# Kernel tuning notes

Hardware: AMD Instinct MI355X
Metric: run time of the kernel (lower is better)

The kernel has to match this reference:

```python
import jax, jax.numpy as jnp
import numpy as np

B, C, H, W = 8, 512, 64, 64
R = 16
CQK = C // R  # 32


def setup_inputs() -> dict:
    key = jax.random.key(0)
    kx, kq, kk, kv = jax.random.split(key, 4)
    x = jax.random.normal(kx, (B, C, H, W), dtype=jnp.float32)
    # Conv1d with kernel_size=1, bias=False == matmul over channel dim
    Wq = jax.random.normal(kq, (CQK, C), dtype=jnp.float32) * (1.0 / np.sqrt(C))
    Wk = jax.random.normal(kk, (CQK, C), dtype=jnp.float32) * (1.0 / np.sqrt(C))
    Wv = jax.random.normal(kv, (C, C), dtype=jnp.float32) * (1.0 / np.sqrt(C))
    return {"x": x, "Wq": Wq, "Wk": Wk, "Wv": Wv}


def reference(x, Wq, Wk, Wv):
    b, c, h, w = x.shape
    xf = x.reshape(b, c, h * w)                 # [b, c, n]
    q = jnp.einsum('dc,bcn->bdn', Wq, xf)       # [b, c/r, n]
    k = jnp.einsum('dc,bcn->bdn', Wk, xf)       # [b, c/r, n]
    attn = jax.nn.softmax(jnp.einsum('bdm,bdn->bmn', q, k), axis=-1)  # [b, n, n]
    v = jnp.einsum('dc,bcn->bdn', Wv, xf)       # [b, c, n]
    out = jnp.einsum('bcm,bmn->bcn', v, attn)   # [b, c, n]
    return out.reshape(b, c, h, w)
```

## Files before the change

### kernel.cpp

```cpp
#include <hip/hip_runtime.h>
#include <hip/hip_bf16.h>


typedef __attribute__((ext_vector_type(8))) short s16x8;
typedef __attribute__((ext_vector_type(4))) float f32x4;

#define MFMA16(a, b, c) __builtin_amdgcn_mfma_f32_16x16x32_bf16((a), (b), (c), 0, 0, 0)

__device__ __forceinline__ ushort f2bf(float f) {
  union { float f; unsigned u; } v; v.f = f;
  return (ushort)((v.u + 0x8000u) >> 16);
}
__device__ __forceinline__ unsigned pack_bf16(float lo, float hi) {
  union { float f; unsigned u; } a, b; a.f = lo; b.f = hi;
  return __builtin_amdgcn_perm(b.u + 0x8000u, a.u + 0x8000u, 0x07060302u);
}
__device__ __forceinline__ float fexp2(float x) { return __builtin_amdgcn_exp2f(x); }

__device__ __forceinline__ void chunk_barrier() {
  asm volatile("s_waitcnt lgkmcnt(0)" ::: "memory");
  __builtin_amdgcn_s_barrier();
  __builtin_amdgcn_sched_barrier(0);
}

__global__ void k_cvt_w(const float* __restrict__ Wq, const float* __restrict__ Wk,
                        const float* __restrict__ Wv, ushort* __restrict__ Wqb,
                        ushort* __restrict__ Wkb, ushort* __restrict__ Wvb) {
  int i = blockIdx.x * 256 + threadIdx.x;
  if (i < 262144) Wvb[i] = f2bf(Wv[i]);
  else if (i < 278528) Wqb[i - 262144] = f2bf(Wq[i - 262144] * 1.4426950408889634f);
  else if (i < 294912) Wkb[i - 278528] = f2bf(Wk[i - 278528]);
}

__global__ __launch_bounds__(256) void k_xpose(const float* __restrict__ x,
                                               ushort* __restrict__ xT) {
  const int b = blockIdx.z, c0 = blockIdx.y * 64, n0 = blockIdx.x * 256;
  __shared__ uint U[2][64][65];
  const int t = threadIdx.x;
  const int wv = t >> 6, ln = t & 63;
  const float* xp = x + ((size_t)b * 512 + c0 + wv * 16) * 4096 + n0 + ln * 4;
#pragma unroll
  for (int i = 0; i < 16; ++i) {
    float4 f = *(const float4*)(xp + (size_t)i * 4096);
    U[0][wv * 16 + i][ln] = pack_bf16(f.x, f.y);
    U[1][wv * 16 + i][ln] = pack_bf16(f.z, f.w);
  }
  __syncthreads();
  const int c_seg = (t & 7) * 8;
#pragma unroll
  for (int pass = 0; pass < 8; ++pass) {
    const int nl = pass * 32 + (t >> 3);
    const int p = nl >> 1;
    const int h = p & 1, idx = p >> 1;
    const uint sel = (nl & 1) ? 0x07060302u : 0x05040100u;
    uint o[4];
#pragma unroll
    for (int j = 0; j < 4; ++j) {
      uint ua = U[h][c_seg + 2 * j][idx];
      uint ub = U[h][c_seg + 2 * j + 1][idx];
      o[j] = __builtin_amdgcn_perm(ub, ua, sel);
    }
    *(uint4*)(xT + ((size_t)b * 4096 + n0 + nl) * 512 + c0 + c_seg) = *(uint4*)o;
  }
}

__global__ __launch_bounds__(256, 2) void k_proj(const ushort* __restrict__ xT,
                                                 const ushort* __restrict__ Wqb,
                                                 const ushort* __restrict__ Wkb,
                                                 const ushort* __restrict__ Wvb,
                                                 ushort* __restrict__ qb,
                                                 ushort* __restrict__ kb,
                                                 ushort* __restrict__ vb) {
  const int b = blockIdx.y, n0 = blockIdx.x * 64;
  const int lane = threadIdx.x & 63, w = threadIdx.x >> 6;
  const int quad = lane >> 4, l15 = lane & 15;
  const ushort* xT_b = xT + (size_t)b * 4096 * 512;

  const ushort* Wqk = (w < 2) ? (Wqb + (size_t)(w * 16 + l15) * 512)
                              : (Wkb + (size_t)((w - 2) * 16 + l15) * 512);

  f32x4 accv[8][4], accqk[4];
#pragma unroll
  for (int i = 0; i < 8; ++i)
#pragma unroll
    for (int nt = 0; nt < 4; ++nt) accv[i][nt] = {0.f, 0.f, 0.f, 0.f};
#pragma unroll
  for (int nt = 0; nt < 4; ++nt) accqk[nt] = {0.f, 0.f, 0.f, 0.f};

  for (int k0 = 0; k0 < 512; k0 += 32) {
    s16x8 bx[4];
#pragma unroll
    for (int nt = 0; nt < 4; ++nt)
      bx[nt] = *(const s16x8*)(xT_b + (size_t)(n0 + nt * 16 + l15) * 512 + k0 + quad * 8);
#pragma unroll
    for (int i = 0; i < 8; ++i) {
      s16x8 av = *(const s16x8*)(Wvb + (size_t)((8 * w + i) * 16 + l15) * 512 + k0 + quad * 8);
#pragma unroll
      for (int nt = 0; nt < 4; ++nt) accv[i][nt] = MFMA16(av, bx[nt], accv[i][nt]);
    }
    s16x8 aqk = *(const s16x8*)(Wqk + k0 + quad * 8);
#pragma unroll
    for (int nt = 0; nt < 4; ++nt) accqk[nt] = MFMA16(aqk, bx[nt], accqk[nt]);
  }

  ushort* vb_b = vb + (size_t)b * 512 * 4096;
#pragma unroll
  for (int i = 0; i < 8; ++i)
#pragma unroll
    for (int nt = 0; nt < 4; ++nt)
#pragma unroll
      for (int r = 0; r < 4; ++r)
        vb_b[(size_t)((8 * w + i) * 16 + quad * 4 + r) * 4096 + n0 + nt * 16 + l15] =
            f2bf(accv[i][nt][r]);

  ushort* qk_out = (w < 2) ? (qb + (size_t)b * 4096 * 32) : (kb + (size_t)b * 4096 * 32);
#pragma unroll
  for (int nt = 0; nt < 4; ++nt) {
    ushort4 u;
    u.x = f2bf(accqk[nt][0]); u.y = f2bf(accqk[nt][1]);
    u.z = f2bf(accqk[nt][2]); u.w = f2bf(accqk[nt][3]);
    *(ushort4*)(qk_out + (size_t)(n0 + nt * 16 + l15) * 32 + (w & 1) * 16 + quad * 4) = u;
  }
}

__global__ __launch_bounds__(256) void k_pass1(const ushort* __restrict__ qb,
                                               const ushort* __restrict__ kb,
                                               float* __restrict__ Lneg) {
  const int b = blockIdx.y, mt = blockIdx.x;
  const int lane = threadIdx.x & 63, w = threadIdx.x >> 6;
  const int quad = lane >> 4, l15 = lane & 15;
  const int m = mt * 64 + w * 16;
  const ushort* qb_b = qb + (size_t)b * 4096 * 32;
  const ushort* kb_b = kb + (size_t)b * 4096 * 32;
  const s16x8 aqf = *(const s16x8*)(qb_b + (size_t)(m + l15) * 32 + quad * 8);
  float ps[4] = {0.f, 0.f, 0.f, 0.f};
  const f32x4 zf = {0.f, 0.f, 0.f, 0.f};
  for (int n0 = 0; n0 < 4096; n0 += 64) {
#pragma unroll
    for (int nt = 0; nt < 4; ++nt) {
      s16x8 bk = *(const s16x8*)(kb_b + (size_t)(n0 + nt * 16 + l15) * 32 + quad * 8);
      f32x4 s = MFMA16(aqf, bk, zf);
#pragma unroll
      for (int r = 0; r < 4; ++r) ps[r] += fexp2(s[r]);
    }
  }
  for (int off = 1; off < 16; off <<= 1)
#pragma unroll
    for (int r = 0; r < 4; ++r) ps[r] += __shfl_xor(ps[r], off, 64);
  if (l15 == 0)
#pragma unroll
    for (int r = 0; r < 4; ++r)
      Lneg[(size_t)b * 4096 + m + quad * 4 + r] = -log2f(ps[r]);
}

__global__ __launch_bounds__(512, 2) void k_pass2(const ushort* __restrict__ qb,
                                                  const ushort* __restrict__ kb,
                                                  const ushort* __restrict__ vb,
                                                  const float* __restrict__ Lneg,
                                                  float* __restrict__ out) {
  const int blk = blockIdx.x;
  const int b = blk & 7, ntb = blk >> 3;
  const int nbase = ntb * 128;
  const int lane = threadIdx.x & 63, w = threadIdx.x >> 6;
  const int quad = lane >> 4, l15 = lane & 15;
  const int cbase = w * 64;
  const int swz = l15 & 7;
  const int Mw = w >> 1;
  const int Tb = (w & 1) * 4;

  __shared__ __align__(16) ushort PT[2][128 * 64];

  const ushort* qb_b = qb + (size_t)b * 4096 * 32;
  const ushort* kb_b = kb + (size_t)b * 4096 * 32;
  const ushort* vb_b = vb + (size_t)b * 512 * 4096;
  const float* L_b = Lneg + (size_t)b * 4096;

  s16x8 kf[4];
#pragma unroll
  for (int i = 0; i < 4; ++i)
    kf[i] = *(const s16x8*)(kb_b + (size_t)(nbase + (Tb + i) * 16 + l15) * 32 + quad * 8);

  f32x4 acc[4][8];
#pragma unroll
  for (int ci = 0; ci < 4; ++ci)
#pragma unroll
    for (int nt = 0; nt < 8; ++nt) acc[ci][nt] = {0.f, 0.f, 0.f, 0.f};

  s16x8 aqp;
  float4 l4p;
  s16x8 va0[4], va1[4];

  auto loadQ = [&](int chunk) {
    const int m0 = chunk * 64;
    aqp = *(const s16x8*)(qb_b + (size_t)(m0 + Mw * 16 + l15) * 32 + quad * 8);
    l4p = *(const float4*)(L_b + m0 + Mw * 16 + quad * 4);
  };
  auto loadV0 = [&](int chunk) {
    const int m0 = chunk * 64;
#pragma unroll
    for (int ci = 0; ci < 4; ++ci)
      va0[ci] = *(const s16x8*)(vb_b + (size_t)(cbase + ci * 16 + l15) * 4096 + m0 + quad * 8);
  };
  auto loadV1 = [&](int chunk) {
    const int m0 = chunk * 64;
#pragma unroll
    for (int ci = 0; ci < 4; ++ci)
      va1[ci] = *(const s16x8*)(vb_b + (size_t)(cbase + ci * 16 + l15) * 4096 + m0 + 32 + quad * 8);
  };
  auto produce_tile = [&](int buf, int i) {
    char* Pw = (char*)&PT[buf][0];
    const int T = Tb + i;
    f32x4 cin; cin.x = l4p.x; cin.y = l4p.y; cin.z = l4p.z; cin.w = l4p.w;
    f32x4 s = MFMA16(aqp, kf[i], cin);
    uint2 u;
    u.x = pack_bf16(fexp2(s.x), fexp2(s.y));
    u.y = pack_bf16(fexp2(s.z), fexp2(s.w));
    const int row = T * 16 + l15;
    const int gran = (2 * Mw + (quad >> 1)) ^ swz;
    *(uint2*)(Pw + row * 128 + gran * 16 + (quad & 1) * 8) = u;
  };

  loadQ(0);
#pragma unroll
  for (int i = 0; i < 4; ++i) produce_tile(0, i);
  loadQ(1);
  loadV0(0);
  loadV1(0);

  for (int chunk = 0; chunk < 64; ++chunk) {
    const int buf = chunk & 1;
    chunk_barrier();
    const char* P = (const char*)&PT[buf][0];
    s16x8 pg[8];
#pragma unroll
    for (int nt = 0; nt < 8; ++nt)
      pg[nt] = *(const s16x8*)(P + (nt * 16 + l15) * 128 + (quad ^ swz) * 16);
#pragma unroll
    for (int i = 0; i < 4; ++i) produce_tile(buf ^ 1, i);
    if (chunk < 62) loadQ(chunk + 2);
    s16x8 rr[8];
#pragma unroll
    for (int nt = 0; nt < 8; ++nt) {
#pragma unroll
      for (int ci = 0; ci < 4; ++ci) acc[ci][nt] = MFMA16(va0[ci], pg[nt], acc[ci][nt]);
      rr[nt] = *(const s16x8*)(P + (nt * 16 + l15) * 128 + ((4 + quad) ^ swz) * 16);
    }
    if (chunk < 63) loadV0(chunk + 1);
#pragma unroll
    for (int nt = 0; nt < 8; ++nt)
#pragma unroll
      for (int ci = 0; ci < 4; ++ci) acc[ci][nt] = MFMA16(va1[ci], rr[nt], acc[ci][nt]);
    if (chunk < 63) loadV1(chunk + 1);
  }

  float* out_b = out + (size_t)b * 512 * 4096;
#pragma unroll
  for (int ci = 0; ci < 4; ++ci)
#pragma unroll
    for (int nt = 0; nt < 8; ++nt) {
      const int n = nbase + nt * 16 + l15;
      const int c0 = cbase + ci * 16 + quad * 4;
#pragma unroll
      for (int r = 0; r < 4; ++r) out_b[(size_t)(c0 + r) * 4096 + n] = acc[ci][nt][r];
    }
}

extern "C" void kernel_launch(void* const* d_in, const int* in_sizes, int n_in,
                              void* d_out, int out_size, void* d_ws, size_t ws_size,
                              hipStream_t stream) {
  const float* x  = (const float*)d_in[0];
  const float* Wq = (const float*)d_in[1];
  const float* Wk = (const float*)d_in[2];
  const float* Wv = (const float*)d_in[3];
  float* out = (float*)d_out;

  char* ws = (char*)d_ws;
  ushort* vb  = (ushort*)(ws + 0);
  ushort* xT  = (ushort*)(ws + 33554432);
  ushort* qb  = (ushort*)(ws + 67108864);
  ushort* kb  = (ushort*)(ws + 69206016);
  ushort* Wvb = (ushort*)(ws + 71303168);
  ushort* Wqb = (ushort*)(ws + 71827456);
  ushort* Wkb = (ushort*)(ws + 71860224);
  float*  Lrs = (float*)(ws + 71892992);

  hipLaunchKernelGGL(k_cvt_w, dim3(1152), dim3(256), 0, stream, Wq, Wk, Wv, Wqb, Wkb, Wvb);
  hipLaunchKernelGGL(k_xpose, dim3(16, 8, 8), dim3(256), 0, stream, x, xT);
  hipLaunchKernelGGL(k_proj, dim3(64, 8), dim3(256), 0, stream, xT, Wqb, Wkb, Wvb, qb, kb, vb);
  hipLaunchKernelGGL(k_pass1, dim3(64, 8), dim3(256), 0, stream, qb, kb, Lrs);
  hipLaunchKernelGGL(k_pass2, dim3(256), dim3(512), 0, stream, qb, kb, vb, Lrs, out);
}
```

Baseline: 346.0 us.

## Split pass2 channel dimension across two blocks with 256-thread workgroups

Pass2 now launches 512 blocks of 256 threads instead of 256 blocks of 512, with each block covering half of the 512 output channels. Each wave now computes two 16-row attention tiles per chunk instead of one, so the exp/softmax tile production is done twice overall (once per channel half). The aim is more blocks to fill the CUs and smaller workgroups with cheaper barriers, at the cost of duplicated QK^T and exp work.

```diff
diff --git a/kernel.cpp b/kernel.cpp
--- a/kernel.cpp
+++ b/kernel.cpp
@@ -153,20 +153,20 @@
       Lneg[(size_t)b * 4096 + m + quad * 4 + r] = -log2f(ps[r]);
 }
 
-__global__ __launch_bounds__(512, 2) void k_pass2(const ushort* __restrict__ qb,
+__global__ __launch_bounds__(256, 2) void k_pass2(const ushort* __restrict__ qb,
                                                   const ushort* __restrict__ kb,
                                                   const ushort* __restrict__ vb,
                                                   const float* __restrict__ Lneg,
                                                   float* __restrict__ out) {
   const int blk = blockIdx.x;
-  const int b = blk & 7, ntb = blk >> 3;
+  const int b = blk & 7, blkb = blk >> 3;
+  const int ntb = blkb & 31, cb = blkb >> 5;
   const int nbase = ntb * 128;
   const int lane = threadIdx.x & 63, w = threadIdx.x >> 6;
   const int quad = lane >> 4, l15 = lane & 15;
-  const int cbase = w * 64;
+  const int wm = w & 1, wn = w >> 1;
+  const int cbase = cb * 256 + w * 64;
   const int swz = l15 & 7;
-  const int Mw = w >> 1;
-  const int Tb = (w & 1) * 4;
 
   __shared__ __align__(16) ushort PT[2][128 * 64];
 
@@ -178,7 +178,7 @@
   s16x8 kf[4];
 #pragma unroll
   for (int i = 0; i < 4; ++i)
-    kf[i] = *(const s16x8*)(kb_b + (size_t)(nbase + (Tb + i) * 16 + l15) * 32 + quad * 8);
+    kf[i] = *(const s16x8*)(kb_b + (size_t)(nbase + (4 * wn + i) * 16 + l15) * 32 + quad * 8);
 
   f32x4 acc[4][8];
 #pragma unroll
@@ -186,14 +186,18 @@
 #pragma unroll
     for (int nt = 0; nt < 8; ++nt) acc[ci][nt] = {0.f, 0.f, 0.f, 0.f};
 
-  s16x8 aqp;
-  float4 l4p;
+  s16x8 aqp[2];
+  float4 l4p[2];
   s16x8 va0[4], va1[4];
 
   auto loadQ = [&](int chunk) {
     const int m0 = chunk * 64;
-    aqp = *(const s16x8*)(qb_b + (size_t)(m0 + Mw * 16 + l15) * 32 + quad * 8);
-    l4p = *(const float4*)(L_b + m0 + Mw * 16 + quad * 4);
+#pragma unroll
+    for (int j = 0; j < 2; ++j) {
+      const int M = 2 * wm + j;
+      aqp[j] = *(const s16x8*)(qb_b + (size_t)(m0 + M * 16 + l15) * 32 + quad * 8);
+      l4p[j] = *(const float4*)(L_b + m0 + M * 16 + quad * 4);
+    }
   };
   auto loadV0 = [&](int chunk) {
     const int m0 = chunk * 64;
@@ -207,22 +211,25 @@
     for (int ci = 0; ci < 4; ++ci)
       va1[ci] = *(const s16x8*)(vb_b + (size_t)(cbase + ci * 16 + l15) * 4096 + m0 + 32 + quad * 8);
   };
-  auto produce_tile = [&](int buf, int i) {
+  auto produce_tile = [&](int buf, int j, int i) {
     char* Pw = (char*)&PT[buf][0];
-    const int T = Tb + i;
-    f32x4 cin; cin.x = l4p.x; cin.y = l4p.y; cin.z = l4p.z; cin.w = l4p.w;
-    f32x4 s = MFMA16(aqp, kf[i], cin);
+    const int M = 2 * wm + j;
+    const int T = 4 * wn + i;
+    f32x4 cin; cin.x = l4p[j].x; cin.y = l4p[j].y; cin.z = l4p[j].z; cin.w = l4p[j].w;
+    f32x4 s = MFMA16(aqp[j], kf[i], cin);
     uint2 u;
     u.x = pack_bf16(fexp2(s.x), fexp2(s.y));
     u.y = pack_bf16(fexp2(s.z), fexp2(s.w));
     const int row = T * 16 + l15;
-    const int gran = (2 * Mw + (quad >> 1)) ^ swz;
+    const int gran = (2 * M + (quad >> 1)) ^ swz;
     *(uint2*)(Pw + row * 128 + gran * 16 + (quad & 1) * 8) = u;
   };
 
   loadQ(0);
 #pragma unroll
-  for (int i = 0; i < 4; ++i) produce_tile(0, i);
+  for (int j = 0; j < 2; ++j)
+#pragma unroll
+    for (int i = 0; i < 4; ++i) produce_tile(0, j, i);
   loadQ(1);
   loadV0(0);
   loadV1(0);
@@ -236,7 +243,9 @@
     for (int nt = 0; nt < 8; ++nt)
       pg[nt] = *(const s16x8*)(P + (nt * 16 + l15) * 128 + (quad ^ swz) * 16);
 #pragma unroll
-    for (int i = 0; i < 4; ++i) produce_tile(buf ^ 1, i);
+    for (int j = 0; j < 2; ++j)
+#pragma unroll
+      for (int i = 0; i < 4; ++i) produce_tile(buf ^ 1, j, i);
     if (chunk < 62) loadQ(chunk + 2);
     s16x8 rr[8];
 #pragma unroll
@@ -288,5 +297,5 @@
   hipLaunchKernelGGL(k_xpose, dim3(16, 8, 8), dim3(256), 0, stream, x, xT);
   hipLaunchKernelGGL(k_proj, dim3(64, 8), dim3(256), 0, stream, xT, Wqb, Wkb, Wvb, qb, kb, vb);
   hipLaunchKernelGGL(k_pass1, dim3(64, 8), dim3(256), 0, stream, qb, kb, Lrs);
-  hipLaunchKernelGGL(k_pass2, dim3(256), dim3(512), 0, stream, qb, kb, vb, Lrs, out);
-}
+  hipLaunchKernelGGL(k_pass2, dim3(512), dim3(256), 0, stream, qb, kb, vb, Lrs, out);
+}
```

Measured after the change: 357.8 us. +3.4%, slower.
